# Kernel optimization log

Hardware: AMD Instinct MI355X
Metric: run time of the kernel (lower is better)

## Reference

```python
import jax, jax.numpy as jnp
import numpy as np

B, N, M, C_PTS, D_MODEL, K = 8, 2048, 8192, 64, 64, 16


def setup_inputs() -> dict:
    key = jax.random.key(0)
    ks = jax.random.split(key, 6)
    xyz = jax.random.normal(ks[0], (B, N, 3), dtype=jnp.float32)
    xyz_fp = jax.random.normal(ks[1], (B, M, 3), dtype=jnp.float32)
    features = jax.random.normal(ks[2], (B, C_PTS, N), dtype=jnp.float32)
    features_fp = jax.random.normal(ks[3], (B, C_PTS, M), dtype=jnp.float32)
    # nn.Linear(d_points, d_model): weight [d_model, d_points], bias [d_model]
    W1 = jax.random.normal(ks[4], (D_MODEL, C_PTS), dtype=jnp.float32) / np.sqrt(C_PTS)
    b1 = jax.random.normal(ks[5], (D_MODEL,), dtype=jnp.float32) * 0.01
    return {"xyz": xyz, "xyz_fp": xyz_fp, "features": features,
            "features_fp": features_fp, "W1": W1, "b1": b1, "k": K}


def reference(xyz, xyz_fp, features, features_fp, W1, b1, k):
    # squared pairwise distances: [B, M, N]
    d2 = jnp.sum((xyz_fp[:, :, None, :] - xyz[:, None, :, :]) ** 2, axis=-1)
    # full argsort then truncate to k (matches torch .argsort()[:, :, :k])
    knn_idx = jnp.argsort(d2, axis=-1)[:, :, :k]              # [B, M, k]
    # index_points(xyz, knn_idx): gather along point axis -> [B, M, k, 3]
    knn_xyz = jax.vmap(lambda pts, idx: pts[idx])(xyz, knn_idx)
    feats = jnp.transpose(features, (0, 2, 1))                # [B, N, d_points]
    _feats_fp = jnp.transpose(features_fp, (0, 2, 1))         # computed, unused (as in source)
    x = feats @ W1.T + b1                                     # [B, N, d_model]
    # Original module returns only `feats`; knn_xyz and x are returned too so
    # the kernel-relevant work (distance + sort + gather + linear) is not DCE'd.
    return feats, knn_xyz, x
```

## Files before the change

kernel.cpp:

```cpp
#include <hip/hip_runtime.h>

#define NB 8
#define NN 2048
#define NM 8192
#define NC 64
#define ND 64
#define NK 16

#define PARTS 8
#define PPT 256
#define CHUNK 260
#define QPB 32
#define NG 8
#define CAP 64
#define CSTR 66

#define KB (NM / QPB)
#define FB (NN / 64)
#define SMEM_BYTES 29312

typedef __attribute__((ext_vector_type(2))) float f2;
typedef __attribute__((ext_vector_type(4))) float f4;

__device__ __forceinline__ int slotOf(int i) {
  const int B = (i & 255) >> 3;
  const int BS = B ^ (B >> 2);
  return (i >> 8) * CHUNK + (BS << 3) + (i & 7);
}

__device__ __forceinline__ float d2rn(float qx, float qy, float qz, float x,
                                      float y, float z) {
  const float dx = __fsub_rn(qx, x);
  const float dy = __fsub_rn(qy, y);
  const float dz = __fsub_rn(qz, z);
  return __fadd_rn(__fadd_rn(__fmul_rn(dx, dx), __fmul_rn(dy, dy)),
                   __fmul_rn(dz, dz));
}

#define CE(a, i, j)                     \
  {                                     \
    const float lo = fminf(a[i], a[j]); \
    const float hi = fmaxf(a[i], a[j]); \
    a[i] = lo;                          \
    a[j] = hi;                          \
  }

#define CEU(a, i, j)                                      \
  {                                                       \
    const bool c_ = a[i] < a[j];                          \
    const unsigned long long lo_ = c_ ? a[i] : a[j];      \
    const unsigned long long hi_ = c_ ? a[j] : a[i];      \
    a[i] = lo_;                                           \
    a[j] = hi_;                                           \
  }

#define SORT8(d)                                  \
  CE(d, 0, 1) CE(d, 2, 3) CE(d, 4, 5) CE(d, 6, 7) \
  CE(d, 0, 2) CE(d, 1, 3) CE(d, 4, 6) CE(d, 5, 7) \
  CE(d, 1, 2) CE(d, 5, 6)                         \
  CE(d, 0, 4) CE(d, 1, 5) CE(d, 2, 6) CE(d, 3, 7) \
  CE(d, 2, 4) CE(d, 3, 5)                         \
  CE(d, 1, 2) CE(d, 3, 4) CE(d, 5, 6)

#define SORT8U(d)                                          \
  CEU(d, 0, 1) CEU(d, 2, 3) CEU(d, 4, 5) CEU(d, 6, 7)      \
  CEU(d, 0, 2) CEU(d, 1, 3) CEU(d, 4, 6) CEU(d, 5, 7)      \
  CEU(d, 1, 2) CEU(d, 5, 6)                                \
  CEU(d, 0, 4) CEU(d, 1, 5) CEU(d, 2, 6) CEU(d, 3, 7)      \
  CEU(d, 2, 4) CEU(d, 3, 5)                                \
  CEU(d, 1, 2) CEU(d, 3, 4) CEU(d, 5, 6)

#define BSORT8U(d)                                         \
  CEU(d, 0, 4) CEU(d, 1, 5) CEU(d, 2, 6) CEU(d, 3, 7)      \
  CEU(d, 0, 2) CEU(d, 1, 3) CEU(d, 4, 6) CEU(d, 5, 7)      \
  CEU(d, 0, 1) CEU(d, 2, 3) CEU(d, 4, 5) CEU(d, 6, 7)

#define BITONIC16(L)                                                      \
  CE(L, 0, 8) CE(L, 1, 9) CE(L, 2, 10) CE(L, 3, 11) CE(L, 4, 12)          \
  CE(L, 5, 13) CE(L, 6, 14) CE(L, 7, 15)                                  \
  CE(L, 0, 4) CE(L, 1, 5) CE(L, 2, 6) CE(L, 3, 7) CE(L, 8, 12)            \
  CE(L, 9, 13) CE(L, 10, 14) CE(L, 11, 15)                                \
  CE(L, 0, 2) CE(L, 1, 3) CE(L, 4, 6) CE(L, 5, 7) CE(L, 8, 10)            \
  CE(L, 9, 11) CE(L, 12, 14) CE(L, 13, 15)                                \
  CE(L, 0, 1) CE(L, 2, 3) CE(L, 4, 5) CE(L, 6, 7) CE(L, 8, 9)             \
  CE(L, 10, 11) CE(L, 12, 13) CE(L, 14, 15)

__device__ __forceinline__ void dist8p(const float* px, const float* py,
                                       const float* pz, int base, float qx,
                                       float qy, float qz, f2 dd[4]) {
#pragma clang fp contract(off)
  const f4 X0 = *(const f4*)&px[base];
  const f4 X1 = *(const f4*)&px[base + 4];
  const f4 Y0 = *(const f4*)&py[base];
  const f4 Y1 = *(const f4*)&py[base + 4];
  const f4 Z0 = *(const f4*)&pz[base];
  const f4 Z1 = *(const f4*)&pz[base + 4];
  const f2 qvx = {qx, qx}, qvy = {qy, qy}, qvz = {qz, qz};
  {
    const f2 dx = qvx - X0.xy, dy = qvy - Y0.xy, dz = qvz - Z0.xy;
    dd[0] = (dx * dx + dy * dy) + dz * dz;
  }
  {
    const f2 dx = qvx - X0.zw, dy = qvy - Y0.zw, dz = qvz - Z0.zw;
    dd[1] = (dx * dx + dy * dy) + dz * dz;
  }
  {
    const f2 dx = qvx - X1.xy, dy = qvy - Y1.xy, dz = qvz - Z1.xy;
    dd[2] = (dx * dx + dy * dy) + dz * dz;
  }
  {
    const f2 dx = qvx - X1.zw, dy = qvy - Y1.zw, dz = qvz - Z1.zw;
    dd[3] = (dx * dx + dy * dy) + dz * dz;
  }
}

__device__ __forceinline__ float min8p(const f2 dd[4]) {
  return fminf(fminf(fminf(dd[0].x, dd[0].y), fminf(dd[1].x, dd[1].y)),
               fminf(fminf(dd[2].x, dd[2].y), fminf(dd[3].x, dd[3].y)));
}

__global__ __launch_bounds__(256, 4) void fused_kernel(
    const float* __restrict__ features, const float* __restrict__ W1,
    const float* __restrict__ b1, float* __restrict__ out_feats,
    float* __restrict__ out_x, const float* __restrict__ xyz,
    const float* __restrict__ xyz_fp, float* __restrict__ out_knn) {
  __shared__ __align__(16) unsigned char smem[SMEM_BYTES];

  const int b = blockIdx.y;
  const int t = threadIdx.x;

  if (blockIdx.x >= KB) {
    float(*tile)[68] = reinterpret_cast<float(*)[68]>(smem);

    const int n0 = (blockIdx.x - KB) * 64;
    const int lane = t & 63;
    const int grp = t >> 6;

    for (int c = grp; c < NC; c += 4)
      tile[c][lane] = features[((size_t)(b * NC + c) * NN) + n0 + lane];

    float4 wreg[16];
    {
      const float4* Wr = (const float4*)(W1 + lane * NC);
#pragma unroll
      for (int k = 0; k < 16; k++) wreg[k] = Wr[k];
    }
    __syncthreads();

    for (int j = grp; j < 64; j += 4)
      out_feats[((size_t)(b * NN + n0 + j) * NC) + lane] = tile[lane][j];

    const int d = lane;
    float acc[16];
    const float bd = b1[d];
#pragma unroll
    for (int jj = 0; jj < 16; jj++) acc[jj] = bd;

    const float4* tv = (const float4*)&tile[0][0];
#pragma unroll
    for (int k = 0; k < 16; k++) {
#pragma unroll
      for (int cc = 0; cc < 4; cc++) {
        const int c = k * 4 + cc;
        const float w = (cc == 0)   ? wreg[k].x
                        : (cc == 1) ? wreg[k].y
                        : (cc == 2) ? wreg[k].z
                                    : wreg[k].w;
#pragma unroll
        for (int q = 0; q < 4; q++) {
          const float4 v = tv[c * 17 + grp * 4 + q];
          acc[q * 4 + 0] = fmaf(v.x, w, acc[q * 4 + 0]);
          acc[q * 4 + 1] = fmaf(v.y, w, acc[q * 4 + 1]);
          acc[q * 4 + 2] = fmaf(v.z, w, acc[q * 4 + 2]);
          acc[q * 4 + 3] = fmaf(v.w, w, acc[q * 4 + 3]);
        }
      }
    }
#pragma unroll
    for (int jj = 0; jj < 16; jj++) {
      const int j = grp * 16 + jj;
      out_x[((size_t)(b * NN + n0 + j) * ND) + d] = acc[jj];
    }
    return;
  }

  float* px = reinterpret_cast<float*>(smem);
  float* py = px + PARTS * CHUNK;
  float* pz = py + PARTS * CHUNK;
  unsigned short* cand =
      reinterpret_cast<unsigned short*>(smem + 3 * PARTS * CHUNK * 4);
  int* ccnt =
      reinterpret_cast<int*>(smem + 3 * PARTS * CHUNK * 4 + QPB * CSTR * 2);

  const int ql = t >> 3;
  const int part = t & 7;

  if (t < QPB) ccnt[t] = 0;

  const float* P = xyz + (size_t)b * NN * 3;
  for (int i = t; i < NN; i += 256) {
    const int slot = slotOf(i);
    px[slot] = P[3 * i + 0];
    py[slot] = P[3 * i + 1];
    pz[slot] = P[3 * i + 2];
  }
  __syncthreads();

  const int q = blockIdx.x * QPB + ql;
  const float* Q = xyz_fp + ((size_t)b * NM + q) * 3;
  const float qx = Q[0], qy = Q[1], qz = Q[2];

  const int pbase = part * CHUNK;

  float gmin[NG];
#pragma unroll
  for (int g = 0; g < NG; g++) {
    float gm = 3.0e38f;
#pragma unroll
    for (int bb = 0; bb < 4; bb++) {
      const int B = g * 4 + bb;
      const int BS = B ^ (B >> 2);
      f2 dd[4];
      dist8p(px, py, pz, pbase + BS * 8, qx, qy, qz, dd);
      gm = fminf(gm, min8p(dd));
    }
    gmin[g] = gm;
  }

  float s[16];
  {
    float g8[NG];
#pragma unroll
    for (int g = 0; g < NG; g++) g8[g] = gmin[g];
    SORT8(g8)
#pragma unroll
    for (int j = 0; j < 8; j++) s[j] = g8[j];
#pragma unroll
    for (int j = 8; j < 16; j++) s[j] = 3.0e38f;
  }
#pragma unroll
  for (int mask = 1; mask <= 4; mask <<= 1) {
    float B[16];
#pragma unroll
    for (int j = 0; j < 16; j++) B[j] = __shfl_xor(s[j], mask, 64);
    float L[16];
#pragma unroll
    for (int j = 0; j < 16; j++) L[j] = fminf(s[j], B[15 - j]);
    BITONIC16(L)
#pragma unroll
    for (int j = 0; j < 16; j++) s[j] = L[j];
  }
  const float T = s[15];

  unsigned m8 = 0;
#pragma unroll
  for (int g = 0; g < NG; g++) m8 |= (gmin[g] <= T) ? (1u << g) : 0u;

  unsigned lo = (part < 4) ? (m8 << (8 * part)) : 0u;
  unsigned hi = (part >= 4) ? (m8 << (8 * (part - 4))) : 0u;
#pragma unroll
  for (int mk = 1; mk <= 4; mk <<= 1) {
    lo |= __shfl_xor(lo, mk, 64);
    hi |= __shfl_xor(hi, mk, 64);
  }
  const unsigned long long vm = ((unsigned long long)hi << 32) | lo;

  unsigned long long mym = 0ull;
  {
    unsigned long long m = vm;
    int cnt = 0;
    while (m) {
      const unsigned long long lb = m & (0ull - m);
      if ((cnt & 7) == part) mym |= lb;
      m ^= lb;
      cnt++;
    }
  }

  while (mym) {
    const int gid = __ffsll(mym) - 1;
    mym &= mym - 1;
    const int cb = (gid >> 3) * CHUNK;
    const int goff = gid & 7;
    const int ib = (gid >> 3) * PPT + goff * 32;
#pragma unroll
    for (int bb = 0; bb < 4; bb++) {
      const int B = goff * 4 + bb;
      const int BS = B ^ (B >> 2);
      f2 dd[4];
      dist8p(px, py, pz, cb + BS * 8, qx, qy, qz, dd);
      if (min8p(dd) <= T) {
        unsigned am = 0;
#pragma unroll
        for (int k = 0; k < 4; k++) {
          am |= (dd[k].x <= T) ? (1u << (2 * k)) : 0u;
          am |= (dd[k].y <= T) ? (1u << (2 * k + 1)) : 0u;
        }
        int pos = atomicAdd(&ccnt[ql], __popc(am));
        while (am) {
          const int k = __ffs(am) - 1;
          am &= am - 1;
          if (pos < CAP)
            cand[ql * CSTR + pos] = (unsigned short)(ib + bb * 8 + k);
          pos++;
        }
      }
    }
  }

  {
    const int cnt = ccnt[ql];
    if (cnt <= CAP) {
      unsigned long long kb8[8];
#pragma unroll
      for (int i = 0; i < 8; i++) {
        const int c = part + 8 * i;
        unsigned long long kk = ~0ULL;
        if (c < cnt) {
          const int idx = cand[ql * CSTR + c];
          const int slot = slotOf(idx);
          const float d2 = d2rn(qx, qy, qz, px[slot], py[slot], pz[slot]);
          kk = ((unsigned long long)__float_as_uint(d2) << 32) | (unsigned)idx;
        }
        kb8[i] = kk;
      }
      SORT8U(kb8)

      {
        unsigned long long bb[8];
#pragma unroll
        for (int j = 0; j < 8; j++) bb[j] = __shfl_xor(kb8[7 - j], 1, 64);
        if (part & 1) {
#pragma unroll
          for (int j = 0; j < 8; j++)
            kb8[j] = (kb8[j] < bb[j]) ? bb[j] : kb8[j];
        } else {
#pragma unroll
          for (int j = 0; j < 8; j++)
            kb8[j] = (kb8[j] < bb[j]) ? kb8[j] : bb[j];
        }
        BSORT8U(kb8)
      }

#pragma unroll
      for (int r = 0; r < 2; r++) {
        const int xm = r ? 5 : 3;
        unsigned long long bb[8];
#pragma unroll
        for (int j = 0; j < 8; j++) bb[j] = __shfl_xor(kb8[7 - j], xm, 64);
#pragma unroll
        for (int j = 0; j < 8; j++)
          kb8[j] = (kb8[j] < bb[j]) ? kb8[j] : bb[j];
#pragma unroll
        for (int j = 0; j < 8; j++) bb[j] = __shfl_xor(kb8[j], 1, 64);
        if (part & 1) {
#pragma unroll
          for (int j = 0; j < 8; j++)
            kb8[j] = (kb8[j] < bb[j]) ? bb[j] : kb8[j];
        } else {
#pragma unroll
          for (int j = 0; j < 8; j++)
            kb8[j] = (kb8[j] < bb[j]) ? kb8[j] : bb[j];
        }
        BSORT8U(kb8)
      }

      if (part < 2) {
#pragma unroll
        for (int j = 0; j < 8; j++)
          cand[ql * CSTR + part * 8 + j] = (unsigned short)(unsigned)kb8[j];
      }
    } else if (part == 0) {
      unsigned long long kb[NK];
#pragma unroll
      for (int j = 0; j < NK; j++) kb[j] = ~0ULL;
      for (int i = 0; i < NN; i++) {
        const int slot = slotOf(i);
        const float d2 = d2rn(qx, qy, qz, px[slot], py[slot], pz[slot]);
        unsigned long long kk =
            ((unsigned long long)__float_as_uint(d2) << 32) | (unsigned)i;
        if (kk < kb[NK - 1]) {
#pragma unroll
          for (int j = 0; j < NK; j++) {
            const bool c2 = kk < kb[j];
            const unsigned long long lo2 = c2 ? kk : kb[j];
            const unsigned long long hi2 = c2 ? kb[j] : kk;
            kb[j] = lo2;
            kk = hi2;
          }
        }
      }
#pragma unroll
      for (int j = 0; j < NK; j++)
        cand[ql * CSTR + j] = (unsigned short)(unsigned)kb[j];
    }
  }

  float* o = out_knn + ((size_t)(b * NM + q)) * (NK * 3);
#pragma unroll
  for (int jj = 0; jj < 2; jj++) {
    const int j = part * 2 + jj;
    const int i = cand[ql * CSTR + j];
    const int slot = slotOf(i);
    o[3 * j + 0] = px[slot];
    o[3 * j + 1] = py[slot];
    o[3 * j + 2] = pz[slot];
  }
}

extern "C" void kernel_launch(void* const* d_in, const int* in_sizes, int n_in,
                              void* d_out, int out_size, void* d_ws,
                              size_t ws_size, hipStream_t stream) {
  const float* xyz      = (const float*)d_in[0];
  const float* xyz_fp   = (const float*)d_in[1];
  const float* features = (const float*)d_in[2];
  const float* W1 = (const float*)d_in[4];
  const float* b1 = (const float*)d_in[5];

  float* out_feats = (float*)d_out;
  float* out_knn   = out_feats + (size_t)NB * NN * NC;
  float* out_x     = out_knn + (size_t)NB * NM * NK * 3;

  fused_kernel<<<dim3(KB + FB, NB), 256, 0, stream>>>(
      features, W1, b1, out_feats, out_x, xyz, xyz_fp, out_knn);
}
```

Measured before the change: 137.0 us.

## Screen KNN candidates in fp16 shared memory, rerank exactly from global fp32

The reference points are stored in shared memory as fp16 and the coarse group-min and candidate filtering run with packed half2 math. The threshold gets a 1% margin so fp16 error is less likely to drop true neighbours. Exact fp32 distances for reranking and the gathered output coordinates now come from global memory. This cuts shared-memory footprint and ALU work, which can raise occupancy. In exchange it adds scattered global loads, and the fixed margin may not hold at every distance scale: fp16 rounding error on coordinates can exceed 1% near small distances.

```diff
diff --git a/kernel.cpp b/kernel.cpp
--- a/kernel.cpp
+++ b/kernel.cpp
@@ -9,7 +9,7 @@
 
 #define PARTS 8
 #define PPT 256
-#define CHUNK 260
+#define HCHUNK 264
 #define QPB 32
 #define NG 8
 #define CAP 64
@@ -17,15 +17,15 @@
 
 #define KB (NM / QPB)
 #define FB (NN / 64)
-#define SMEM_BYTES 29312
-
-typedef __attribute__((ext_vector_type(2))) float f2;
-typedef __attribute__((ext_vector_type(4))) float f4;
+#define SMEM_BYTES 17408
+
+typedef __attribute__((ext_vector_type(2))) _Float16 h2;
+typedef __attribute__((ext_vector_type(8))) _Float16 h8;
 
 __device__ __forceinline__ int slotOf(int i) {
   const int B = (i & 255) >> 3;
   const int BS = B ^ (B >> 2);
-  return (i >> 8) * CHUNK + (BS << 3) + (i & 7);
+  return (i >> 8) * HCHUNK + (BS << 3) + (i & 7);
 }
 
 __device__ __forceinline__ float d2rn(float qx, float qy, float qz, float x,
@@ -85,38 +85,28 @@
   CE(L, 0, 1) CE(L, 2, 3) CE(L, 4, 5) CE(L, 6, 7) CE(L, 8, 9)             \
   CE(L, 10, 11) CE(L, 12, 13) CE(L, 14, 15)
 
-__device__ __forceinline__ void dist8p(const float* px, const float* py,
-                                       const float* pz, int base, float qx,
-                                       float qy, float qz, f2 dd[4]) {
-#pragma clang fp contract(off)
-  const f4 X0 = *(const f4*)&px[base];
-  const f4 X1 = *(const f4*)&px[base + 4];
-  const f4 Y0 = *(const f4*)&py[base];
-  const f4 Y1 = *(const f4*)&py[base + 4];
-  const f4 Z0 = *(const f4*)&pz[base];
-  const f4 Z1 = *(const f4*)&pz[base + 4];
-  const f2 qvx = {qx, qx}, qvy = {qy, qy}, qvz = {qz, qz};
-  {
-    const f2 dx = qvx - X0.xy, dy = qvy - Y0.xy, dz = qvz - Z0.xy;
-    dd[0] = (dx * dx + dy * dy) + dz * dz;
-  }
-  {
-    const f2 dx = qvx - X0.zw, dy = qvy - Y0.zw, dz = qvz - Z0.zw;
-    dd[1] = (dx * dx + dy * dy) + dz * dz;
-  }
-  {
-    const f2 dx = qvx - X1.xy, dy = qvy - Y1.xy, dz = qvz - Z1.xy;
-    dd[2] = (dx * dx + dy * dy) + dz * dz;
-  }
-  {
-    const f2 dx = qvx - X1.zw, dy = qvy - Y1.zw, dz = qvz - Z1.zw;
-    dd[3] = (dx * dx + dy * dy) + dz * dz;
-  }
-}
-
-__device__ __forceinline__ float min8p(const f2 dd[4]) {
-  return fminf(fminf(fminf(dd[0].x, dd[0].y), fminf(dd[1].x, dd[1].y)),
-               fminf(fminf(dd[2].x, dd[2].y), fminf(dd[3].x, dd[3].y)));
+__device__ __forceinline__ void dist8h(const _Float16* hx, const _Float16* hy,
+                                       const _Float16* hz, int base, h2 qvx,
+                                       h2 qvy, h2 qvz, h2 dd[4]) {
+  const h8 X = *(const h8*)&hx[base];
+  const h8 Y = *(const h8*)&hy[base];
+  const h8 Z = *(const h8*)&hz[base];
+#pragma unroll
+  for (int k = 0; k < 4; k++) {
+    const h2 xk = {X[2 * k], X[2 * k + 1]};
+    const h2 yk = {Y[2 * k], Y[2 * k + 1]};
+    const h2 zk = {Z[2 * k], Z[2 * k + 1]};
+    const h2 dx = qvx - xk, dy = qvy - yk, dz = qvz - zk;
+    dd[k] = __builtin_elementwise_fma(
+        dz, dz, __builtin_elementwise_fma(dy, dy, dx * dx));
+  }
+}
+
+__device__ __forceinline__ float min8h(const h2 dd[4]) {
+  const h2 m = __builtin_elementwise_min(
+      __builtin_elementwise_min(dd[0], dd[1]),
+      __builtin_elementwise_min(dd[2], dd[3]));
+  return fminf((float)m[0], (float)m[1]);
 }
 
 __global__ __launch_bounds__(256, 4) void fused_kernel(
@@ -184,13 +174,13 @@
     return;
   }
 
-  float* px = reinterpret_cast<float*>(smem);
-  float* py = px + PARTS * CHUNK;
-  float* pz = py + PARTS * CHUNK;
+  _Float16* hx = reinterpret_cast<_Float16*>(smem);
+  _Float16* hy = hx + PARTS * HCHUNK;
+  _Float16* hz = hy + PARTS * HCHUNK;
   unsigned short* cand =
-      reinterpret_cast<unsigned short*>(smem + 3 * PARTS * CHUNK * 4);
+      reinterpret_cast<unsigned short*>(smem + 3 * PARTS * HCHUNK * 2);
   int* ccnt =
-      reinterpret_cast<int*>(smem + 3 * PARTS * CHUNK * 4 + QPB * CSTR * 2);
+      reinterpret_cast<int*>(smem + 3 * PARTS * HCHUNK * 2 + QPB * CSTR * 2);
 
   const int ql = t >> 3;
   const int part = t & 7;
@@ -200,31 +190,36 @@
   const float* P = xyz + (size_t)b * NN * 3;
   for (int i = t; i < NN; i += 256) {
     const int slot = slotOf(i);
-    px[slot] = P[3 * i + 0];
-    py[slot] = P[3 * i + 1];
-    pz[slot] = P[3 * i + 2];
+    hx[slot] = (_Float16)P[3 * i + 0];
+    hy[slot] = (_Float16)P[3 * i + 1];
+    hz[slot] = (_Float16)P[3 * i + 2];
   }
   __syncthreads();
 
   const int q = blockIdx.x * QPB + ql;
   const float* Q = xyz_fp + ((size_t)b * NM + q) * 3;
   const float qx = Q[0], qy = Q[1], qz = Q[2];
-
-  const int pbase = part * CHUNK;
+  const _Float16 qhx = (_Float16)qx, qhy = (_Float16)qy, qhz = (_Float16)qz;
+  const h2 qvx = {qhx, qhx}, qvy = {qhy, qhy}, qvz = {qhz, qhz};
+
+  const int pbase = part * HCHUNK;
 
   float gmin[NG];
 #pragma unroll
   for (int g = 0; g < NG; g++) {
-    float gm = 3.0e38f;
+    h2 gm2 = {(_Float16)6.0e4f, (_Float16)6.0e4f};
 #pragma unroll
     for (int bb = 0; bb < 4; bb++) {
       const int B = g * 4 + bb;
       const int BS = B ^ (B >> 2);
-      f2 dd[4];
-      dist8p(px, py, pz, pbase + BS * 8, qx, qy, qz, dd);
-      gm = fminf(gm, min8p(dd));
-    }
-    gmin[g] = gm;
+      h2 dd[4];
+      dist8h(hx, hy, hz, pbase + BS * 8, qvx, qvy, qvz, dd);
+      gm2 = __builtin_elementwise_min(
+          gm2, __builtin_elementwise_min(
+                   __builtin_elementwise_min(dd[0], dd[1]),
+                   __builtin_elementwise_min(dd[2], dd[3])));
+    }
+    gmin[g] = fminf((float)gm2[0], (float)gm2[1]);
   }
 
   float s[16];
@@ -250,11 +245,11 @@
 #pragma unroll
     for (int j = 0; j < 16; j++) s[j] = L[j];
   }
-  const float T = s[15];
+  const float Te = s[15] * 1.01f;
 
   unsigned m8 = 0;
 #pragma unroll
-  for (int g = 0; g < NG; g++) m8 |= (gmin[g] <= T) ? (1u << g) : 0u;
+  for (int g = 0; g < NG; g++) m8 |= (gmin[g] <= Te) ? (1u << g) : 0u;
 
   unsigned lo = (part < 4) ? (m8 << (8 * part)) : 0u;
   unsigned hi = (part >= 4) ? (m8 << (8 * (part - 4))) : 0u;
@@ -280,21 +275,21 @@
   while (mym) {
     const int gid = __ffsll(mym) - 1;
     mym &= mym - 1;
-    const int cb = (gid >> 3) * CHUNK;
+    const int cb = (gid >> 3) * HCHUNK;
     const int goff = gid & 7;
     const int ib = (gid >> 3) * PPT + goff * 32;
 #pragma unroll
     for (int bb = 0; bb < 4; bb++) {
       const int B = goff * 4 + bb;
       const int BS = B ^ (B >> 2);
-      f2 dd[4];
-      dist8p(px, py, pz, cb + BS * 8, qx, qy, qz, dd);
-      if (min8p(dd) <= T) {
+      h2 dd[4];
+      dist8h(hx, hy, hz, cb + BS * 8, qvx, qvy, qvz, dd);
+      if (min8h(dd) <= Te) {
         unsigned am = 0;
 #pragma unroll
         for (int k = 0; k < 4; k++) {
-          am |= (dd[k].x <= T) ? (1u << (2 * k)) : 0u;
-          am |= (dd[k].y <= T) ? (1u << (2 * k + 1)) : 0u;
+          am |= ((float)dd[k][0] <= Te) ? (1u << (2 * k)) : 0u;
+          am |= ((float)dd[k][1] <= Te) ? (1u << (2 * k + 1)) : 0u;
         }
         int pos = atomicAdd(&ccnt[ql], __popc(am));
         while (am) {
@@ -318,8 +313,8 @@
         unsigned long long kk = ~0ULL;
         if (c < cnt) {
           const int idx = cand[ql * CSTR + c];
-          const int slot = slotOf(idx);
-          const float d2 = d2rn(qx, qy, qz, px[slot], py[slot], pz[slot]);
+          const float d2 = d2rn(qx, qy, qz, P[3 * idx], P[3 * idx + 1],
+                                P[3 * idx + 2]);
           kk = ((unsigned long long)__float_as_uint(d2) << 32) | (unsigned)idx;
         }
         kb8[i] = kk;
@@ -375,8 +370,8 @@
 #pragma unroll
       for (int j = 0; j < NK; j++) kb[j] = ~0ULL;
       for (int i = 0; i < NN; i++) {
-        const int slot = slotOf(i);
-        const float d2 = d2rn(qx, qy, qz, px[slot], py[slot], pz[slot]);
+        const float d2 =
+            d2rn(qx, qy, qz, P[3 * i], P[3 * i + 1], P[3 * i + 2]);
         unsigned long long kk =
             ((unsigned long long)__float_as_uint(d2) << 32) | (unsigned)i;
         if (kk < kb[NK - 1]) {
@@ -401,10 +396,9 @@
   for (int jj = 0; jj < 2; jj++) {
     const int j = part * 2 + jj;
     const int i = cand[ql * CSTR + j];
-    const int slot = slotOf(i);
-    o[3 * j + 0] = px[slot];
-    o[3 * j + 1] = py[slot];
-    o[3 * j + 2] = pz[slot];
+    o[3 * j + 0] = P[3 * i + 0];
+    o[3 * j + 1] = P[3 * i + 1];
+    o[3 * j + 2] = P[3 * i + 2];
   }
 }
 
```

Result: no change. 135.1 us (-1.4%).
